# Kernel optimization log

Measured on AMD Instinct MI355X. Metric: run time of the kernel, lower is better.

Reference implementation:

```python
import jax, jax.numpy as jnp
import numpy as np

TEMPERATURE = 0.07
EPS = 1e-8


def setup_inputs() -> dict:
    key = jax.random.key(0)
    k1, k2 = jax.random.split(key)
    B, T, D = 512, 196, 256
    text_tokens = jax.random.normal(k1, (B, T, D), dtype=jnp.float32)
    visual_tokens = jax.random.normal(k2, (B, T, D), dtype=jnp.float32)
    return {"text_tokens": text_tokens, "visual_tokens": visual_tokens}


def reference(text_tokens, visual_tokens):
    # text_tokens, visual_tokens: [B, T, D]
    B = text_tokens.shape[0]
    # Per-token norms [B, T]
    tnorm = jnp.linalg.norm(text_tokens, axis=-1)
    vnorm = jnp.linalg.norm(visual_tokens, axis=-1)
    # Pairwise token dot products, same token index t: [B, B, T]
    dots = jnp.einsum('btd,ctd->bct', text_tokens, visual_tokens)
    # torch cosine_similarity: dot / max(|x|*|y|, eps)
    denom = jnp.maximum(tnorm[:, None, :] * vnorm[None, :, :], EPS)
    cos = dots / denom  # [B, B, T]
    # Softmax pooling over tokens
    w = jax.nn.softmax(cos, axis=-1)
    sim = jnp.sum(cos * w, axis=-1)  # [B, B]
    logits = sim / TEMPERATURE
    # Bidirectional InfoNCE with diagonal labels
    lsm_t2i = jax.nn.log_softmax(logits, axis=-1)
    lsm_i2t = jax.nn.log_softmax(logits.T, axis=-1)
    diag = jnp.arange(B)
    loss_t2i = -jnp.mean(lsm_t2i[diag, diag])
    loss_i2t = -jnp.mean(lsm_i2t[diag, diag])
    loss = 0.5 * (loss_t2i + loss_i2t)
    return loss
```

## Files before the change

kernel.cpp:

```cpp
#include <hip/hip_runtime.h>

#define BB 512
#define TTOK 196
#define DD 256
#define TCHUNK 14
#define NCHUNK 14
#define BM 64
#define BK 64
#define NSTAGE (TCHUNK * 4)

typedef __attribute__((ext_vector_type(8))) __bf16 bf16x8;
typedef __attribute__((ext_vector_type(4))) float floatx4;
typedef __attribute__((address_space(3))) char* lds_t;
typedef const __attribute__((address_space(1))) void* gas_t;

__device__ __forceinline__ unsigned short f2bf(float f) {
  unsigned int u = __float_as_uint(f);
  u += 0x7FFFu + ((u >> 16) & 1u);
  return (unsigned short)(u >> 16);
}

__global__ __launch_bounds__(256) void k_norm2(const float* __restrict__ text,
                                               const float* __restrict__ visual,
                                               unsigned short* __restrict__ An,
                                               unsigned short* __restrict__ Vn) {
  const float* in = blockIdx.y ? visual : text;
  unsigned short* out = blockIdx.y ? Vn : An;
  int u = blockIdx.x * 4 + threadIdx.y;
  int lane = threadIdx.x;
  int b = u / TTOK;
  int t = u - b * TTOK;
  float4 v = *((const float4*)(in + (size_t)u * DD) + lane);
  float ss = v.x * v.x + v.y * v.y + v.z * v.z + v.w * v.w;
#pragma unroll
  for (int off = 32; off; off >>= 1) ss += __shfl_xor(ss, off, 64);
  float inv = ss > 1e-24f ? 1.0f / sqrtf(ss) : 0.0f;
  ushort4 o;
  o.x = f2bf(v.x * inv);
  o.y = f2bf(v.y * inv);
  o.z = f2bf(v.z * inv);
  o.w = f2bf(v.w * inv);
  *((ushort4*)(out + ((size_t)t * BB + b) * DD) + lane) = o;
}

__global__ __launch_bounds__(256, 4) void k_gemm_pool(
    const unsigned short* __restrict__ An, const unsigned short* __restrict__ Vn,
    float2* __restrict__ partial) {
  __shared__ char smem[32768];
  const int tid = threadIdx.x;
  const int wave = tid >> 6, lane = tid & 63;
  const int wr = wave >> 1, wc = wave & 1;
  const int lm = lane & 15, quad = lane >> 4, l7 = lane & 7;
  const int row_base = blockIdx.x * BM;
  const int col_base = blockIdx.y * BM;
  const int t0 = blockIdx.z * TCHUNK;

  unsigned aoffs[2], boffs[2];
#pragma unroll
  for (int q = 0; q < 2; q++) {
    int s = q * 256 + tid;
    int r = s >> 3;
    int g = (s & 7) ^ (r & 7);
    aoffs[q] = (unsigned)(row_base + r) * DD + (unsigned)g * 8;
    boffs[q] = (unsigned)(col_base + r) * DD + (unsigned)g * 8;
  }
  lds_t lds = (lds_t)smem;
  const unsigned ldsoff = (unsigned)tid * 16u;

  unsigned aRow[2], bRow[2];
#pragma unroll
  for (int i = 0; i < 2; i++) {
    aRow[i] = (unsigned)(wr * 32 + i * 16 + lm) * 128u;
    bRow[i] = (unsigned)(wc * 32 + i * 16 + lm) * 128u;
  }

  floatx4 acc[2][2], sacc[2][2], wacc[2][2];
#pragma unroll
  for (int i = 0; i < 2; i++)
#pragma unroll
    for (int j = 0; j < 2; j++) {
      acc[i][j] = (floatx4){0.f, 0.f, 0.f, 0.f};
      sacc[i][j] = (floatx4){0.f, 0.f, 0.f, 0.f};
      wacc[i][j] = (floatx4){0.f, 0.f, 0.f, 0.f};
    }

  auto issue = [&](int st, int buf) {
    int t = t0 + (st >> 2);
    unsigned kb = (unsigned)(st & 3) * BK;
    const unsigned short* Ab = An + (size_t)t * (BB * DD) + kb;
    const unsigned short* Bb = Vn + (size_t)t * (BB * DD) + kb;
    unsigned lb = (unsigned)buf * 16384u + ldsoff;
#pragma unroll
    for (int q = 0; q < 2; q++)
      __builtin_amdgcn_global_load_lds((gas_t)(Ab + aoffs[q]),
                                       (__attribute__((address_space(3))) void*)(lds + lb + (unsigned)q * 4096u),
                                       16, 0, 0);
#pragma unroll
    for (int q = 0; q < 2; q++)
      __builtin_amdgcn_global_load_lds((gas_t)(Bb + boffs[q]),
                                       (__attribute__((address_space(3))) void*)(lds + lb + 8192u + (unsigned)q * 4096u),
                                       16, 0, 0);
  };

  issue(0, 0);
  for (int st = 0; st < NSTAGE; ++st) {
    int buf = st & 1;
    __syncthreads();
    if (st + 1 < NSTAGE) issue(st + 1, buf ^ 1);
    const char* A = smem + buf * 16384;
    const char* B = smem + buf * 16384 + 8192;
#pragma unroll
    for (int k0 = 0; k0 < BK; k0 += 32) {
      unsigned gsw = (unsigned)((((k0 >> 3) + quad) ^ l7)) * 16u;
      bf16x8 a[2], b[2];
#pragma unroll
      for (int mi = 0; mi < 2; mi++) a[mi] = *(const bf16x8*)(A + aRow[mi] + gsw);
#pragma unroll
      for (int ni = 0; ni < 2; ni++) b[ni] = *(const bf16x8*)(B + bRow[ni] + gsw);
#pragma unroll
      for (int mi = 0; mi < 2; mi++)
#pragma unroll
        for (int ni = 0; ni < 2; ni++)
          acc[mi][ni] = __builtin_amdgcn_mfma_f32_16x16x32_bf16(a[mi], b[ni], acc[mi][ni], 0, 0, 0);
    }
    if ((st & 3) == 3) {
#pragma unroll
      for (int mi = 0; mi < 2; mi++)
#pragma unroll
        for (int ni = 0; ni < 2; ni++) {
#pragma unroll
          for (int r = 0; r < 4; r++) {
            float c = acc[mi][ni][r];
            float e = __expf(c - 1.0f);
            sacc[mi][ni][r] += e;
            wacc[mi][ni][r] = fmaf(c, e, wacc[mi][ni][r]);
          }
          acc[mi][ni] = (floatx4){0.f, 0.f, 0.f, 0.f};
        }
    }
  }

  size_t cb = (size_t)blockIdx.z * (BB * BB);
#pragma unroll
  for (int mi = 0; mi < 2; mi++) {
    int bi = row_base + wr * 32 + mi * 16 + quad * 4;
#pragma unroll
    for (int r = 0; r < 4; r++)
#pragma unroll
      for (int ni = 0; ni < 2; ni++) {
        int ci = col_base + wc * 32 + ni * 16 + lm;
        partial[cb + (size_t)(bi + r) * BB + ci] = make_float2(sacc[mi][ni][r], wacc[mi][ni][r]);
      }
  }
}

__global__ __launch_bounds__(256) void k_merge(const float2* __restrict__ partial,
                                               float* __restrict__ logits) {
  int idx = blockIdx.x * 256 + threadIdx.x;
  float s = 0.f, w = 0.f;
#pragma unroll
  for (int ch = 0; ch < NCHUNK; ++ch) {
    float2 p = partial[(size_t)ch * (BB * BB) + idx];
    s += p.x;
    w += p.y;
  }
  logits[idx] = (w / s) * (1.0f / 0.07f);
}

__global__ __launch_bounds__(256) void k_lse(const float* __restrict__ logits,
                                             float* __restrict__ contrib) {
  int b = blockIdx.x;
  int tid = threadIdx.x;
  __shared__ float sm[4];

  float r0 = logits[(size_t)b * BB + tid];
  float r1 = logits[(size_t)b * BB + tid + 256];
  float c0 = logits[(size_t)tid * BB + b];
  float c1 = logits[((size_t)tid + 256) * BB + b];

  float v = fmaxf(r0, r1);
#pragma unroll
  for (int off = 32; off; off >>= 1) v = fmaxf(v, __shfl_xor(v, off, 64));
  if ((tid & 63) == 0) sm[tid >> 6] = v;
  __syncthreads();
  float mr = fmaxf(fmaxf(sm[0], sm[1]), fmaxf(sm[2], sm[3]));
  __syncthreads();
  v = __expf(r0 - mr) + __expf(r1 - mr);
#pragma unroll
  for (int off = 32; off; off >>= 1) v += __shfl_xor(v, off, 64);
  if ((tid & 63) == 0) sm[tid >> 6] = v;
  __syncthreads();
  float sr = sm[0] + sm[1] + sm[2] + sm[3];
  __syncthreads();
  v = fmaxf(c0, c1);
#pragma unroll
  for (int off = 32; off; off >>= 1) v = fmaxf(v, __shfl_xor(v, off, 64));
  if ((tid & 63) == 0) sm[tid >> 6] = v;
  __syncthreads();
  float mc = fmaxf(fmaxf(sm[0], sm[1]), fmaxf(sm[2], sm[3]));
  __syncthreads();
  v = __expf(c0 - mc) + __expf(c1 - mc);
#pragma unroll
  for (int off = 32; off; off >>= 1) v += __shfl_xor(v, off, 64);
  if ((tid & 63) == 0) sm[tid >> 6] = v;
  __syncthreads();
  float sc = sm[0] + sm[1] + sm[2] + sm[3];

  if (tid == 0) {
    float diag = logits[(size_t)b * BB + b];
    contrib[b] = 2.f * diag - (mr + logf(sr)) - (mc + logf(sc));
  }
}

__global__ __launch_bounds__(256) void k_final(const float* __restrict__ contrib,
                                               float* __restrict__ out) {
  int tid = threadIdx.x;
  float v = contrib[tid] + contrib[tid + 256];
#pragma unroll
  for (int off = 32; off; off >>= 1) v += __shfl_xor(v, off, 64);
  __shared__ float sm[4];
  if ((tid & 63) == 0) sm[tid >> 6] = v;
  __syncthreads();
  if (tid == 0) out[0] = -(sm[0] + sm[1] + sm[2] + sm[3]) * (1.0f / 1024.0f);
}

extern "C" void kernel_launch(void* const* d_in, const int* in_sizes, int n_in,
                              void* d_out, int out_size, void* d_ws, size_t ws_size,
                              hipStream_t stream) {
  const float* text = (const float*)d_in[0];
  const float* visual = (const float*)d_in[1];

  char* ws = (char*)d_ws;
  const size_t szN = (size_t)TTOK * BB * DD * sizeof(unsigned short);
  const size_t szP = (size_t)NCHUNK * BB * BB * sizeof(float2);
  unsigned short* An = (unsigned short*)ws;
  unsigned short* Vn = (unsigned short*)(ws + szN);
  float2* partial = (float2*)(ws + 2 * szN);
  float* logits = (float*)(ws + 2 * szN + szP);
  float* contrib = (float*)(ws + 2 * szN + szP + (size_t)BB * BB * sizeof(float));

  dim3 blk1(64, 4);
  k_norm2<<<dim3(BB * TTOK / 4, 2), blk1, 0, stream>>>(text, visual, An, Vn);
  k_gemm_pool<<<dim3(8, 8, NCHUNK), 256, 0, stream>>>(An, Vn, partial);
  k_merge<<<BB * BB / 256, 256, 0, stream>>>(partial, logits);
  k_lse<<<BB, 256, 0, stream>>>(logits, contrib);
  k_final<<<1, 256, 0, stream>>>(contrib, (float*)d_out);
}
```

Baseline: 310.8 us.

## Widen GEMM tile to 64x128, keep natural token layout, remap blocks per XCD

The normalization kernel now writes bf16 tokens in their original [B,T,D] order instead of transposing to [T,B,D], and the GEMM reads rows with a T*D stride. The GEMM tile grows from 64x64 to 64x128 (each wave does 2x4 MFMA tiles), which halves the grid and raises reuse of A loads, at the cost of more LDS (48KB) and registers with occupancy lowered to 3. Block indices are remapped so that each XCD handles a contiguous range of tiles, with the goal of improving L2 locality. Strided row reads may hurt coalescing per load, but each row still covers 128 contiguous bytes.

```diff
diff --git a/kernel.cpp b/kernel.cpp
--- a/kernel.cpp
+++ b/kernel.cpp
@@ -3,9 +3,9 @@
 #define BB 512
 #define TTOK 196
 #define DD 256
+#define ROWSTRIDE (TTOK * DD)
 #define TCHUNK 14
 #define NCHUNK 14
-#define BM 64
 #define BK 64
 #define NSTAGE (TCHUNK * 4)
 
@@ -28,8 +28,6 @@
   unsigned short* out = blockIdx.y ? Vn : An;
   int u = blockIdx.x * 4 + threadIdx.y;
   int lane = threadIdx.x;
-  int b = u / TTOK;
-  int t = u - b * TTOK;
   float4 v = *((const float4*)(in + (size_t)u * DD) + lane);
   float ss = v.x * v.x + v.y * v.y + v.z * v.z + v.w * v.w;
 #pragma unroll
@@ -40,94 +38,106 @@
   o.y = f2bf(v.y * inv);
   o.z = f2bf(v.z * inv);
   o.w = f2bf(v.w * inv);
-  *((ushort4*)(out + ((size_t)t * BB + b) * DD) + lane) = o;
-}
-
-__global__ __launch_bounds__(256, 4) void k_gemm_pool(
+  *((ushort4*)(out + (size_t)u * DD) + lane) = o;
+}
+
+__global__ __launch_bounds__(256, 3) void k_gemm_pool(
     const unsigned short* __restrict__ An, const unsigned short* __restrict__ Vn,
     float2* __restrict__ partial) {
-  __shared__ char smem[32768];
+  __shared__ char smem[49152];
   const int tid = threadIdx.x;
   const int wave = tid >> 6, lane = tid & 63;
   const int wr = wave >> 1, wc = wave & 1;
   const int lm = lane & 15, quad = lane >> 4, l7 = lane & 7;
-  const int row_base = blockIdx.x * BM;
-  const int col_base = blockIdx.y * BM;
-  const int t0 = blockIdx.z * TCHUNK;
-
-  unsigned aoffs[2], boffs[2];
+
+  int flat = blockIdx.x + 8 * blockIdx.y + 32 * blockIdx.z;
+  int xcd = flat & 7, j = flat >> 3;
+  int virt = xcd * 56 + j;
+  int vz = virt >> 5;
+  int rst = virt & 31;
+  int vy = rst >> 3, vx = rst & 7;
+  const int row_base = vx * 64;
+  const int col_base = vy * 128;
+  const int t0 = vz * TCHUNK;
+
+  unsigned aoffs[2], boffs[4];
 #pragma unroll
   for (int q = 0; q < 2; q++) {
     int s = q * 256 + tid;
     int r = s >> 3;
     int g = (s & 7) ^ (r & 7);
-    aoffs[q] = (unsigned)(row_base + r) * DD + (unsigned)g * 8;
-    boffs[q] = (unsigned)(col_base + r) * DD + (unsigned)g * 8;
+    aoffs[q] = (unsigned)(row_base + r) * ROWSTRIDE + (unsigned)g * 8;
+  }
+#pragma unroll
+  for (int q = 0; q < 4; q++) {
+    int s = q * 256 + tid;
+    int r = s >> 3;
+    int g = (s & 7) ^ (r & 7);
+    boffs[q] = (unsigned)(col_base + r) * ROWSTRIDE + (unsigned)g * 8;
   }
   lds_t lds = (lds_t)smem;
   const unsigned ldsoff = (unsigned)tid * 16u;
 
-  unsigned aRow[2], bRow[2];
-#pragma unroll
-  for (int i = 0; i < 2; i++) {
-    aRow[i] = (unsigned)(wr * 32 + i * 16 + lm) * 128u;
-    bRow[i] = (unsigned)(wc * 32 + i * 16 + lm) * 128u;
-  }
-
-  floatx4 acc[2][2], sacc[2][2], wacc[2][2];
+  floatx4 acc[2][4], sacc[2][4], wacc[2][4];
 #pragma unroll
   for (int i = 0; i < 2; i++)
 #pragma unroll
-    for (int j = 0; j < 2; j++) {
-      acc[i][j] = (floatx4){0.f, 0.f, 0.f, 0.f};
-      sacc[i][j] = (floatx4){0.f, 0.f, 0.f, 0.f};
-      wacc[i][j] = (floatx4){0.f, 0.f, 0.f, 0.f};
+    for (int n = 0; n < 4; n++) {
+      acc[i][n] = (floatx4){0.f, 0.f, 0.f, 0.f};
+      sacc[i][n] = (floatx4){0.f, 0.f, 0.f, 0.f};
+      wacc[i][n] = (floatx4){0.f, 0.f, 0.f, 0.f};
     }
 
   auto issue = [&](int st, int buf) {
     int t = t0 + (st >> 2);
     unsigned kb = (unsigned)(st & 3) * BK;
-    const unsigned short* Ab = An + (size_t)t * (BB * DD) + kb;
-    const unsigned short* Bb = Vn + (size_t)t * (BB * DD) + kb;
-    unsigned lb = (unsigned)buf * 16384u + ldsoff;
+    const unsigned short* Ab = An + (size_t)t * DD + kb;
+    const unsigned short* Bb = Vn + (size_t)t * DD + kb;
+    unsigned lb = (unsigned)buf * 24576u + ldsoff;
 #pragma unroll
     for (int q = 0; q < 2; q++)
       __builtin_amdgcn_global_load_lds((gas_t)(Ab + aoffs[q]),
                                        (__attribute__((address_space(3))) void*)(lds + lb + (unsigned)q * 4096u),
                                        16, 0, 0);
 #pragma unroll
-    for (int q = 0; q < 2; q++)
+    for (int q = 0; q < 4; q++)
       __builtin_amdgcn_global_load_lds((gas_t)(Bb + boffs[q]),
                                        (__attribute__((address_space(3))) void*)(lds + lb + 8192u + (unsigned)q * 4096u),
                                        16, 0, 0);
   };
+
+  unsigned aRow[2], bRow[4];
+#pragma unroll
+  for (int i = 0; i < 2; i++) aRow[i] = (unsigned)(wr * 32 + i * 16 + lm) * 128u;
+#pragma unroll
+  for (int n = 0; n < 4; n++) bRow[n] = (unsigned)(wc * 64 + n * 16 + lm) * 128u;
 
   issue(0, 0);
   for (int st = 0; st < NSTAGE; ++st) {
     int buf = st & 1;
     __syncthreads();
     if (st + 1 < NSTAGE) issue(st + 1, buf ^ 1);
-    const char* A = smem + buf * 16384;
-    const char* B = smem + buf * 16384 + 8192;
+    const char* A = smem + buf * 24576;
+    const char* B = A + 8192;
 #pragma unroll
     for (int k0 = 0; k0 < BK; k0 += 32) {
-      unsigned gsw = (unsigned)((((k0 >> 3) + quad) ^ l7)) * 16u;
-      bf16x8 a[2], b[2];
+      unsigned gsw = (unsigned)(((k0 >> 3) + quad) ^ l7) * 16u;
+      bf16x8 a[2], b[4];
 #pragma unroll
       for (int mi = 0; mi < 2; mi++) a[mi] = *(const bf16x8*)(A + aRow[mi] + gsw);
 #pragma unroll
-      for (int ni = 0; ni < 2; ni++) b[ni] = *(const bf16x8*)(B + bRow[ni] + gsw);
+      for (int ni = 0; ni < 4; ni++) b[ni] = *(const bf16x8*)(B + bRow[ni] + gsw);
 #pragma unroll
       for (int mi = 0; mi < 2; mi++)
 #pragma unroll
-        for (int ni = 0; ni < 2; ni++)
+        for (int ni = 0; ni < 4; ni++)
           acc[mi][ni] = __builtin_amdgcn_mfma_f32_16x16x32_bf16(a[mi], b[ni], acc[mi][ni], 0, 0, 0);
     }
     if ((st & 3) == 3) {
 #pragma unroll
       for (int mi = 0; mi < 2; mi++)
 #pragma unroll
-        for (int ni = 0; ni < 2; ni++) {
+        for (int ni = 0; ni < 4; ni++) {
 #pragma unroll
           for (int r = 0; r < 4; r++) {
             float c = acc[mi][ni][r];
@@ -140,15 +150,15 @@
     }
   }
 
-  size_t cb = (size_t)blockIdx.z * (BB * BB);
+  size_t cb = (size_t)vz * (BB * BB);
 #pragma unroll
   for (int mi = 0; mi < 2; mi++) {
     int bi = row_base + wr * 32 + mi * 16 + quad * 4;
 #pragma unroll
     for (int r = 0; r < 4; r++)
 #pragma unroll
-      for (int ni = 0; ni < 2; ni++) {
-        int ci = col_base + wc * 32 + ni * 16 + lm;
+      for (int ni = 0; ni < 4; ni++) {
+        int ci = col_base + wc * 64 + ni * 16 + lm;
         partial[cb + (size_t)(bi + r) * BB + ci] = make_float2(sacc[mi][ni][r], wacc[mi][ni][r]);
       }
   }
@@ -241,7 +251,7 @@
 
   dim3 blk1(64, 4);
   k_norm2<<<dim3(BB * TTOK / 4, 2), blk1, 0, stream>>>(text, visual, An, Vn);
-  k_gemm_pool<<<dim3(8, 8, NCHUNK), 256, 0, stream>>>(An, Vn, partial);
+  k_gemm_pool<<<dim3(8, 4, NCHUNK), 256, 0, stream>>>(An, Vn, partial);
   k_merge<<<BB * BB / 256, 256, 0, stream>>>(partial, logits);
   k_lse<<<BB, 256, 0, stream>>>(logits, contrib);
   k_final<<<1, 256, 0, stream>>>(contrib, (float*)d_out);
```

New measurement: 291.4 us. 1.07x faster.
